# Kernel tuning notes

Hardware: AMD Instinct MI355X
Metric: run time of the kernel (lower is better)

## Reference

```python
import jax, jax.numpy as jnp
import numpy as np

N_NODES, N_EDGES, D_FEAT, HIDDEN, N_CLASSES = 100000, 3200000, 128, 16, 40


def setup_inputs() -> dict:
    key = jax.random.key(0)
    ks = jax.random.split(key, 6)
    x = jax.random.normal(ks[0], (N_NODES, D_FEAT), dtype=jnp.float32)
    edge_index = jax.random.randint(ks[1], (2, N_EDGES), 0, N_NODES, dtype=jnp.int32)
    # SAGEConv params: lin_l (aggregated neighbors, with bias), lin_r (root, no bias)
    W_l = jax.random.normal(ks[2], (D_FEAT, HIDDEN), dtype=jnp.float32) / np.sqrt(D_FEAT)
    b_l = jnp.zeros((HIDDEN,), jnp.float32)
    W_r = jax.random.normal(ks[3], (D_FEAT, HIDDEN), dtype=jnp.float32) / np.sqrt(D_FEAT)
    # final Linear(hidden, num_classes)
    W3 = jax.random.normal(ks[4], (HIDDEN, N_CLASSES), dtype=jnp.float32) / np.sqrt(HIDDEN)
    b3 = jnp.zeros((N_CLASSES,), jnp.float32)
    return {"x": x, "edge_index": edge_index, "W_l": W_l, "b_l": b_l,
            "W_r": W_r, "W3": W3, "b3": b3}


def reference(x, edge_index, W_l, b_l, W_r, W3, b3):
    N = x.shape[0]
    src, dst = edge_index[0], edge_index[1]
    # mean aggregation of source features onto target nodes (PyG source_to_target)
    agg = jax.ops.segment_sum(x[src], dst, num_segments=N)            # [N, F]
    deg = jax.ops.segment_sum(jnp.ones_like(dst, dtype=x.dtype), dst, num_segments=N)
    mean = agg / jnp.maximum(deg, 1.0)[:, None]                        # zero-in-degree -> 0
    # SAGEConv: lin_l(mean) + lin_r(x)
    h = mean @ W_l + b_l + x @ W_r                                     # [N, 16]
    h = jax.nn.relu(h)
    logits = h @ W3 + b3                                               # [N, C]
    return jax.nn.log_softmax(logits, axis=1)
```

## Files before the change

### kernel.cpp

```cpp
#include <hip/hip_runtime.h>
#include <hip/hip_bf16.h>

#define D_FEAT 128
#define HIDDEN 16
#define NCLS 40
#define EPB 4096
#define QSCALE 32.0f
#define QBIAS  8.0f

typedef unsigned int uint;

__global__ __launch_bounds__(256) void p1lin_kernel(
    const int* __restrict__ src, const int* __restrict__ dst,
    int* __restrict__ gcur1, int* __restrict__ buf1,
    int E, int C, int R1, int nb1,
    const float* __restrict__ x,
    const float* __restrict__ Wl, const float* __restrict__ Wr,
    uint* __restrict__ ylb, float* __restrict__ yr, int N) {
  __shared__ __align__(16) char smem[33280];
  int tid = threadIdx.x;

  if (blockIdx.x < nb1) {
    int* lh    = (int*)smem;
    int* loff  = lh + 32;
    int* gbase = loff + 32;
    int* lbuf  = gbase + 32;
    int* ldst  = lbuf + 4096;
    if (tid < 32) lh[tid] = 0;
    __syncthreads();

    int base = blockIdx.x * EPB;
    int key[16], rnk[16], rec[16];
#pragma unroll
    for (int j = 0; j < 16; ++j) {
      int e = base + j * 256 + tid;
      bool ok = e < E;
      int d = ok ? dst[e] : 0;
      int s = ok ? src[e] : 0;
      key[j] = ok ? (d >> 12) : -1;
      rec[j] = s | ((d & 4095) << 17);
      if (ok) rnk[j] = atomicAdd(&lh[key[j]], 1);
    }
    __syncthreads();

    if (tid < 64) {
      int v = (tid < 32) ? lh[tid] : 0;
      int inc = v;
#pragma unroll
      for (int dd = 1; dd < 32; dd <<= 1) {
        int t = __shfl_up(inc, dd);
        if ((int)tid >= dd) inc += t;
      }
      if (tid < 32) {
        loff[tid] = inc - v;
        gbase[tid] = (v && tid < C) ? atomicAdd(&gcur1[tid], v) : 0;
      }
    }
    __syncthreads();

#pragma unroll
    for (int j = 0; j < 16; ++j) {
      if (key[j] >= 0) {
        int p = loff[key[j]] + rnk[j];
        lbuf[p] = rec[j];
        int gp = gbase[key[j]] + rnk[j];
        ldst[p] = (gp < R1) ? key[j] * R1 + gp : -1;
      }
    }
    __syncthreads();

    int tot = min(EPB, E - base);
    for (int i = tid; i < tot; i += 256) {
      int di = ldst[i];
      if (di >= 0) buf1[di] = lbuf[i];
    }
  } else {
    float (*sW)[8][4] = (float(*)[8][4])smem;
    float (*sx)[132]  = (float(*)[132])(smem + 16384);

    for (int idx = tid; idx < D_FEAT * 32; idx += 256) {
      int k = idx >> 5, o = idx & 31;
      float v = (o < 16) ? Wl[k * 16 + o] : Wr[k * 16 + (o - 16)];
      sW[k][o >> 2][o & 3] = v;
    }

    int row0 = (blockIdx.x - nb1) * 32;
    for (int q = tid; q < 32 * 32; q += 256) {
      int r = q >> 5, k4 = q & 31;
      int row = row0 + r;
      float4 v = make_float4(0.f, 0.f, 0.f, 0.f);
      if (row < N) v = *(const float4*)(x + (size_t)row * D_FEAT + k4 * 4);
      *(float4*)(&sx[r][k4 * 4]) = v;
    }
    __syncthreads();

    int r = tid >> 3, oq = tid & 7;
    int row = row0 + r;
    if (row < N) {
      float4 acc = make_float4(0.f, 0.f, 0.f, 0.f);
#pragma unroll
      for (int k = 0; k < D_FEAT; ++k) {
        float xv = sx[r][k];
        const float4 w = *(const float4*)(&sW[k][oq][0]);
        acc.x += xv * w.x; acc.y += xv * w.y;
        acc.z += xv * w.z; acc.w += xv * w.w;
      }
      if (oq < 4) {
        int q0 = __float2int_rn((fminf(fmaxf(acc.x, -7.9f), 7.9f) + QBIAS) * QSCALE);
        int q1 = __float2int_rn((fminf(fmaxf(acc.y, -7.9f), 7.9f) + QBIAS) * QSCALE);
        int q2 = __float2int_rn((fminf(fmaxf(acc.z, -7.9f), 7.9f) + QBIAS) * QSCALE);
        int q3 = __float2int_rn((fminf(fmaxf(acc.w, -7.9f), 7.9f) + QBIAS) * QSCALE);
        uint2 pk;
        pk.x = (uint)q0 | ((uint)q1 << 16);
        pk.y = (uint)q2 | ((uint)q3 << 16);
        *(uint2*)(ylb + (size_t)row * 8 + oq * 2) = pk;
      } else {
        *(float4*)(yr + (size_t)row * 16 + (oq - 4) * 4) = acc;
      }
    }
  }
}

__global__ __launch_bounds__(256) void pass2_kernel(
    const int* __restrict__ buf1, const int* __restrict__ gcur1,
    int* __restrict__ gcur, int* __restrict__ packed,
    int C, int R1, int RF, int chunks) {
  int c = blockIdx.x / chunks;
  int chunk = blockIdx.x - c * chunks;
  int cnt1 = min(gcur1[c], R1);
  int base = chunk * EPB;
  int tot = cnt1 - base;
  if (tot <= 0) return;
  tot = min(tot, EPB);

  __shared__ int lh[32], loff[32], gbase[32];
  __shared__ int lbuf[EPB];
  __shared__ int ldst[EPB];
  int tid = threadIdx.x;
  if (tid < 32) lh[tid] = 0;
  __syncthreads();

  const int* in = buf1 + (size_t)c * R1 + base;
  int key[16], rnk[16], rec[16];
#pragma unroll
  for (int j = 0; j < 16; ++j) {
    int i = j * 256 + tid;
    bool ok = i < tot;
    int r = ok ? in[i] : 0;
    int d12 = (r >> 17) & 4095;
    key[j] = ok ? (d12 >> 7) : -1;
    rec[j] = (r & 0x1FFFF) | ((d12 & 127) << 20);
    if (ok) rnk[j] = atomicAdd(&lh[key[j]], 1);
  }
  __syncthreads();

  if (tid < 64) {
    int v = (tid < 32) ? lh[tid] : 0;
    int inc = v;
#pragma unroll
    for (int dd = 1; dd < 32; dd <<= 1) {
      int t = __shfl_up(inc, dd);
      if ((int)tid >= dd) inc += t;
    }
    if (tid < 32) {
      loff[tid] = inc - v;
      gbase[tid] = v ? atomicAdd(&gcur[c * 32 + tid], v) : 0;
    }
  }
  __syncthreads();

#pragma unroll
  for (int j = 0; j < 16; ++j) {
    if (key[j] >= 0) {
      int p = loff[key[j]] + rnk[j];
      lbuf[p] = rec[j];
      int gp = gbase[key[j]] + rnk[j];
      ldst[p] = (gp < RF) ? (c * 32 + key[j]) * RF + gp : -1;
    }
  }
  __syncthreads();

  for (int i = tid; i < tot; i += 256) {
    int di = ldst[i];
    if (di >= 0) packed[di] = lbuf[i];
  }
}

__global__ __launch_bounds__(1024) void baggrf_kernel(
    const uint* __restrict__ ylb, const int* __restrict__ packed,
    const int* __restrict__ gcur, const float* __restrict__ yr,
    const float* __restrict__ bl, const float* __restrict__ W3,
    const float* __restrict__ b3, float* __restrict__ out,
    int N, int RF) {
  __shared__ uint sagg[128 * 9];
  __shared__ int sdeg[128];
  __shared__ float syr[128 * 16];
  __shared__ float sW3[16 * NCLS];
  __shared__ float sb3[NCLS];
  __shared__ float sbl[16];
  int tid = threadIdx.x;
  int b = blockIdx.x;
  int node0 = b * 128;

  for (int i = tid; i < 128 * 9; i += 1024) sagg[i] = 0u;
  if (tid < 128) sdeg[tid] = 0;
  if (tid >= 384 && tid < 1024) sW3[tid - 384] = W3[tid - 384];
  if (tid < NCLS) sb3[tid] = b3[tid];
  if (tid >= 64 && tid < 80) sbl[tid - 64] = bl[tid - 64];
  __syncthreads();

  int cnt = min(gcur[b], RF);
  int lo = b * RF, hi = lo + cnt;
  for (int e = lo + tid; e < hi; e += 2048) {
    int eb = e + 1024;
    bool has2 = eb < hi;
    int p0 = packed[e];
    int p1 = packed[has2 ? eb : e];
    int s0 = p0 & 0xFFFFF, d0 = (p0 >> 20) & 127;
    int s1 = p1 & 0xFFFFF, d1 = (p1 >> 20) & 127;
    const uint4* q0 = (const uint4*)(ylb + (size_t)s0 * 8);
    const uint4* q1 = (const uint4*)(ylb + (size_t)s1 * 8);
    uint4 a0 = q0[0], a1 = q0[1];
    uint4 b0 = q1[0], b1 = q1[1];

    uint* ip0 = &sagg[d0 * 9];
    atomicAdd(ip0 + 0, a0.x); atomicAdd(ip0 + 1, a0.y);
    atomicAdd(ip0 + 2, a0.z); atomicAdd(ip0 + 3, a0.w);
    atomicAdd(ip0 + 4, a1.x); atomicAdd(ip0 + 5, a1.y);
    atomicAdd(ip0 + 6, a1.z); atomicAdd(ip0 + 7, a1.w);
    atomicAdd(&sdeg[d0], 1);
    if (has2) {
      uint* ip1 = &sagg[d1 * 9];
      atomicAdd(ip1 + 0, b0.x); atomicAdd(ip1 + 1, b0.y);
      atomicAdd(ip1 + 2, b0.z); atomicAdd(ip1 + 3, b0.w);
      atomicAdd(ip1 + 4, b1.x); atomicAdd(ip1 + 5, b1.y);
      atomicAdd(ip1 + 6, b1.z); atomicAdd(ip1 + 7, b1.w);
      atomicAdd(&sdeg[d1], 1);
    }
  }

  int nvalid = min(128, N - node0);
  if (nvalid > 0) {
    int tot16 = nvalid * 16;
    for (int i = tid; i < tot16; i += 1024)
      syr[i] = yr[(size_t)node0 * 16 + i];
  }
  __syncthreads();

  int node = tid >> 3, q = tid & 7;
  int n = node0 + node;
  if (n < N) {
    int dg = sdeg[node];
    float bsub = (QBIAS * QSCALE) * (float)dg;
    float inv = 1.0f / (QSCALE * fmaxf((float)dg, 1.0f));
    float h[16];
#pragma unroll
    for (int j = 0; j < 8; ++j) {
      uint s = sagg[node * 9 + j];
      float v0 = ((float)(s & 0xFFFFu) - bsub) * inv;
      float v1 = ((float)(s >> 16) - bsub) * inv;
      h[2 * j]     = fmaxf(v0 + sbl[2 * j]     + syr[node * 16 + 2 * j], 0.f);
      h[2 * j + 1] = fmaxf(v1 + sbl[2 * j + 1] + syr[node * 16 + 2 * j + 1], 0.f);
    }
    float lg[5];
#pragma unroll
    for (int j = 0; j < 5; ++j) lg[j] = sb3[q * 5 + j];
#pragma unroll
    for (int k = 0; k < 16; ++k) {
      float hv = h[k];
#pragma unroll
      for (int j = 0; j < 5; ++j) lg[j] += hv * sW3[k * NCLS + q * 5 + j];
    }
    float m = lg[0];
#pragma unroll
    for (int j = 1; j < 5; ++j) m = fmaxf(m, lg[j]);
#pragma unroll
    for (int dd = 1; dd < 8; dd <<= 1) m = fmaxf(m, __shfl_xor(m, dd));
    float s = 0.f;
#pragma unroll
    for (int j = 0; j < 5; ++j) s += __expf(lg[j] - m);
#pragma unroll
    for (int dd = 1; dd < 8; dd <<= 1) s += __shfl_xor(s, dd);
    float lse = m + __logf(s);
    float* op = out + (size_t)n * NCLS + q * 5;
#pragma unroll
    for (int j = 0; j < 5; ++j) op[j] = lg[j] - lse;
  }
}

extern "C" void kernel_launch(void* const* d_in, const int* in_sizes, int n_in,
                              void* d_out, int out_size, void* d_ws, size_t ws_size,
                              hipStream_t stream) {
  const float* x   = (const float*)d_in[0];
  const int* eidx  = (const int*)d_in[1];
  const float* Wl  = (const float*)d_in[2];
  const float* bl  = (const float*)d_in[3];
  const float* Wr  = (const float*)d_in[4];
  const float* W3  = (const float*)d_in[5];
  const float* b3  = (const float*)d_in[6];
  float* out = (float*)d_out;

  int N = in_sizes[0] / D_FEAT;
  int E = in_sizes[1] / 2;
  const int* src = eidx;
  const int* dst = eidx + E;

  int C = (N + 4095) >> 12;
  int chunks = (E / C) / EPB + 2;
  int R1 = chunks * EPB;
  int Bf = C * 32;
  int B = (N + 127) >> 7;
  long long m = (long long)E * 128 / N;
  int RF = (int)((m + m / 8 + 511) / 512 * 512);

  size_t n16 = (size_t)N * 16;
  uint* ylb   = (uint*)d_ws;
  float* yr   = (float*)(ylb + (size_t)N * 8);
  int* gcur   = (int*)(yr + n16);
  int* gcur1  = gcur + Bf;
  int* buf1   = gcur1 + C;
  int* packed = buf1 + (size_t)C * R1;

  hipMemsetAsync(gcur, 0, (size_t)(Bf + C) * sizeof(int), stream);

  int nb1 = (E + EPB - 1) / EPB;
  int nblin = (N + 31) / 32;
  p1lin_kernel<<<nb1 + nblin, 256, 0, stream>>>(src, dst, gcur1, buf1,
                                                E, C, R1, nb1,
                                                x, Wl, Wr, ylb, yr, N);

  pass2_kernel<<<C * chunks, 256, 0, stream>>>(buf1, gcur1, gcur, packed,
                                               C, R1, RF, chunks);

  baggrf_kernel<<<B, 1024, 0, stream>>>(ylb, packed, gcur, yr, bl, W3, b3,
                                        out, N, RF);
}
```

Baseline: 95.92 us.

## Fold counter zeroing into first kernel, slim pass2 scatter, unroll aggregation by four

Replaces the separate memset with zeroing by block 0 of the first kernel, published through a release flag that other partitioning blocks spin on before their global atomics. The flag is reset at the start of the final kernel. Pass2 now keeps only the record buffer in shared memory and recomputes the destination index at scatter time, which cuts its shared memory use. The aggregation loop issues four edge gathers per iteration instead of two, giving more memory-level parallelism. The spin-wait assumes block 0 is scheduled and makes progress, and the flag starts out uninitialised on the very first call.

```diff
diff --git a/kernel.cpp b/kernel.cpp
--- a/kernel.cpp
+++ b/kernel.cpp
@@ -7,20 +7,28 @@
 #define EPB 4096
 #define QSCALE 32.0f
 #define QBIAS  8.0f
+#define RELEASE 0x5A17C0DE
 
 typedef unsigned int uint;
 
 __global__ __launch_bounds__(256) void p1lin_kernel(
     const int* __restrict__ src, const int* __restrict__ dst,
-    int* __restrict__ gcur1, int* __restrict__ buf1,
-    int E, int C, int R1, int nb1,
+    int* __restrict__ gcur, int* __restrict__ gcur1, int* __restrict__ flag,
+    int* __restrict__ buf1, int E, int C, int R1, int nb1, int nzero,
     const float* __restrict__ x,
     const float* __restrict__ Wl, const float* __restrict__ Wr,
     uint* __restrict__ ylb, float* __restrict__ yr, int N) {
   __shared__ __align__(16) char smem[33280];
   int tid = threadIdx.x;
 
-  if (blockIdx.x < nb1) {
+  if ((int)blockIdx.x == 0) {
+    for (int i = tid; i < nzero; i += 256) gcur[i] = 0;
+    __threadfence();
+    __syncthreads();
+    if (tid == 0) atomicExch(flag, RELEASE);
+  }
+
+  if ((int)blockIdx.x < nb1) {
     int* lh    = (int*)smem;
     int* loff  = lh + 32;
     int* gbase = loff + 32;
@@ -43,6 +51,12 @@
     }
     __syncthreads();
 
+    if (tid == 0) {
+      while (atomicCAS(flag, RELEASE, RELEASE) != RELEASE) {}
+    }
+    __syncthreads();
+    __threadfence();
+
     if (tid < 64) {
       int v = (tid < 32) ? lh[tid] : 0;
       int inc = v;
@@ -84,7 +98,7 @@
       sW[k][o >> 2][o & 3] = v;
     }
 
-    int row0 = (blockIdx.x - nb1) * 32;
+    int row0 = ((int)blockIdx.x - nb1) * 32;
     for (int q = tid; q < 32 * 32; q += 256) {
       int r = q >> 5, k4 = q & 31;
       int row = row0 + r;
@@ -125,6 +139,9 @@
     const int* __restrict__ buf1, const int* __restrict__ gcur1,
     int* __restrict__ gcur, int* __restrict__ packed,
     int C, int R1, int RF, int chunks) {
+  __shared__ int lbuf[EPB];
+  __shared__ int lh[32], loff[32], gbase[32];
+
   int c = blockIdx.x / chunks;
   int chunk = blockIdx.x - c * chunks;
   int cnt1 = min(gcur1[c], R1);
@@ -133,9 +150,6 @@
   if (tot <= 0) return;
   tot = min(tot, EPB);
 
-  __shared__ int lh[32], loff[32], gbase[32];
-  __shared__ int lbuf[EPB];
-  __shared__ int ldst[EPB];
   int tid = threadIdx.x;
   if (tid < 32) lh[tid] = 0;
   __syncthreads();
@@ -147,9 +161,8 @@
     int i = j * 256 + tid;
     bool ok = i < tot;
     int r = ok ? in[i] : 0;
-    int d12 = (r >> 17) & 4095;
-    key[j] = ok ? (d12 >> 7) : -1;
-    rec[j] = (r & 0x1FFFF) | ((d12 & 127) << 20);
+    key[j] = ok ? ((r >> 24) & 31) : -1;
+    rec[j] = r;
     if (ok) rnk[j] = atomicAdd(&lh[key[j]], 1);
   }
   __syncthreads();
@@ -170,19 +183,19 @@
   __syncthreads();
 
 #pragma unroll
-  for (int j = 0; j < 16; ++j) {
-    if (key[j] >= 0) {
-      int p = loff[key[j]] + rnk[j];
-      lbuf[p] = rec[j];
-      int gp = gbase[key[j]] + rnk[j];
-      ldst[p] = (gp < RF) ? (c * 32 + key[j]) * RF + gp : -1;
-    }
-  }
+  for (int j = 0; j < 16; ++j)
+    if (key[j] >= 0) lbuf[loff[key[j]] + rnk[j]] = rec[j];
   __syncthreads();
 
   for (int i = tid; i < tot; i += 256) {
-    int di = ldst[i];
-    if (di >= 0) packed[di] = lbuf[i];
+    int r = lbuf[i];
+    int k = (r >> 24) & 31;
+    int gp = gbase[k] + (i - loff[k]);
+    if (gp < RF) {
+      int d12 = (r >> 17) & 4095;
+      packed[(size_t)(c * 32 + k) * RF + gp] =
+          (r & 0x1FFFF) | ((d12 & 127) << 20);
+    }
   }
 }
 
@@ -191,7 +204,7 @@
     const int* __restrict__ gcur, const float* __restrict__ yr,
     const float* __restrict__ bl, const float* __restrict__ W3,
     const float* __restrict__ b3, float* __restrict__ out,
-    int N, int RF) {
+    int* __restrict__ flag, int N, int RF) {
   __shared__ uint sagg[128 * 9];
   __shared__ int sdeg[128];
   __shared__ float syr[128 * 16];
@@ -202,6 +215,8 @@
   int b = blockIdx.x;
   int node0 = b * 128;
 
+  if (b == 0 && tid == 0) atomicExch(flag, 0);
+
   for (int i = tid; i < 128 * 9; i += 1024) sagg[i] = 0u;
   if (tid < 128) sdeg[tid] = 0;
   if (tid >= 384 && tid < 1024) sW3[tid - 384] = W3[tid - 384];
@@ -211,17 +226,25 @@
 
   int cnt = min(gcur[b], RF);
   int lo = b * RF, hi = lo + cnt;
-  for (int e = lo + tid; e < hi; e += 2048) {
-    int eb = e + 1024;
-    bool has2 = eb < hi;
-    int p0 = packed[e];
-    int p1 = packed[has2 ? eb : e];
+  for (int e0 = lo + tid; e0 < hi; e0 += 4096) {
+    int e1 = e0 + 1024, e2 = e0 + 2048, e3 = e0 + 3072;
+    bool h1 = e1 < hi, h2 = e2 < hi, h3 = e3 < hi;
+    int p0 = packed[e0];
+    int p1 = packed[h1 ? e1 : e0];
+    int p2 = packed[h2 ? e2 : e0];
+    int p3 = packed[h3 ? e3 : e0];
     int s0 = p0 & 0xFFFFF, d0 = (p0 >> 20) & 127;
     int s1 = p1 & 0xFFFFF, d1 = (p1 >> 20) & 127;
+    int s2 = p2 & 0xFFFFF, d2 = (p2 >> 20) & 127;
+    int s3 = p3 & 0xFFFFF, d3 = (p3 >> 20) & 127;
     const uint4* q0 = (const uint4*)(ylb + (size_t)s0 * 8);
     const uint4* q1 = (const uint4*)(ylb + (size_t)s1 * 8);
+    const uint4* q2 = (const uint4*)(ylb + (size_t)s2 * 8);
+    const uint4* q3 = (const uint4*)(ylb + (size_t)s3 * 8);
     uint4 a0 = q0[0], a1 = q0[1];
     uint4 b0 = q1[0], b1 = q1[1];
+    uint4 c0 = q2[0], c1 = q2[1];
+    uint4 e4 = q3[0], e5 = q3[1];
 
     uint* ip0 = &sagg[d0 * 9];
     atomicAdd(ip0 + 0, a0.x); atomicAdd(ip0 + 1, a0.y);
@@ -229,13 +252,29 @@
     atomicAdd(ip0 + 4, a1.x); atomicAdd(ip0 + 5, a1.y);
     atomicAdd(ip0 + 6, a1.z); atomicAdd(ip0 + 7, a1.w);
     atomicAdd(&sdeg[d0], 1);
-    if (has2) {
-      uint* ip1 = &sagg[d1 * 9];
-      atomicAdd(ip1 + 0, b0.x); atomicAdd(ip1 + 1, b0.y);
-      atomicAdd(ip1 + 2, b0.z); atomicAdd(ip1 + 3, b0.w);
-      atomicAdd(ip1 + 4, b1.x); atomicAdd(ip1 + 5, b1.y);
-      atomicAdd(ip1 + 6, b1.z); atomicAdd(ip1 + 7, b1.w);
+    if (h1) {
+      uint* ip = &sagg[d1 * 9];
+      atomicAdd(ip + 0, b0.x); atomicAdd(ip + 1, b0.y);
+      atomicAdd(ip + 2, b0.z); atomicAdd(ip + 3, b0.w);
+      atomicAdd(ip + 4, b1.x); atomicAdd(ip + 5, b1.y);
+      atomicAdd(ip + 6, b1.z); atomicAdd(ip + 7, b1.w);
       atomicAdd(&sdeg[d1], 1);
+    }
+    if (h2) {
+      uint* ip = &sagg[d2 * 9];
+      atomicAdd(ip + 0, c0.x); atomicAdd(ip + 1, c0.y);
+      atomicAdd(ip + 2, c0.z); atomicAdd(ip + 3, c0.w);
+      atomicAdd(ip + 4, c1.x); atomicAdd(ip + 5, c1.y);
+      atomicAdd(ip + 6, c1.z); atomicAdd(ip + 7, c1.w);
+      atomicAdd(&sdeg[d2], 1);
+    }
+    if (h3) {
+      uint* ip = &sagg[d3 * 9];
+      atomicAdd(ip + 0, e4.x); atomicAdd(ip + 1, e4.y);
+      atomicAdd(ip + 2, e4.z); atomicAdd(ip + 3, e4.w);
+      atomicAdd(ip + 4, e5.x); atomicAdd(ip + 5, e5.y);
+      atomicAdd(ip + 6, e5.z); atomicAdd(ip + 7, e5.w);
+      atomicAdd(&sdeg[d3], 1);
     }
   }
 
@@ -320,18 +359,18 @@
   int* gcur1  = gcur + Bf;
   int* buf1   = gcur1 + C;
   int* packed = buf1 + (size_t)C * R1;
-
-  hipMemsetAsync(gcur, 0, (size_t)(Bf + C) * sizeof(int), stream);
+  int* flag   = packed + (size_t)Bf * RF;
 
   int nb1 = (E + EPB - 1) / EPB;
   int nblin = (N + 31) / 32;
-  p1lin_kernel<<<nb1 + nblin, 256, 0, stream>>>(src, dst, gcur1, buf1,
-                                                E, C, R1, nb1,
+  int nzero = Bf + C;
+  p1lin_kernel<<<nb1 + nblin, 256, 0, stream>>>(src, dst, gcur, gcur1, flag,
+                                                buf1, E, C, R1, nb1, nzero,
                                                 x, Wl, Wr, ylb, yr, N);
 
   pass2_kernel<<<C * chunks, 256, 0, stream>>>(buf1, gcur1, gcur, packed,
                                                C, R1, RF, chunks);
 
   baggrf_kernel<<<B, 1024, 0, stream>>>(ylb, packed, gcur, yr, bl, W3, b3,
-                                        out, N, RF);
+                                        out, flag, N, RF);
 }
```

After: 139.6 us. 45.6% more time.
